# Kernel tuning notes

Hardware: AMD Instinct MI355X
Metric: run time of the kernel (lower is better)

The kernel has to match this reference:

```python
import jax, jax.numpy as jnp
import numpy as np

N = 100000
E = 1600000
IN_FEATS = 256
OUT_FEATS = 128
THRESHOLD = 0.5


def setup_inputs() -> dict:
    key = jax.random.key(0)
    k1, k2, k3, k4, k5, k6, k7 = jax.random.split(key, 7)
    return {
        "feat": jax.random.normal(k1, (N, IN_FEATS), dtype=jnp.float32),
        "src": jax.random.randint(k2, (E,), 0, N, dtype=jnp.int32),
        "dst": jax.random.randint(k3, (E,), 0, N, dtype=jnp.int32),
        "edge_weight": jax.random.uniform(k4, (E,), dtype=jnp.float32),
        "weight": jax.random.normal(k5, (IN_FEATS, OUT_FEATS), dtype=jnp.float32),
        "bias": jax.random.normal(k6, (OUT_FEATS,), dtype=jnp.float32),
        "mask_real": jax.random.uniform(k7, (IN_FEATS, OUT_FEATS), dtype=jnp.float32),
    }


def reference(feat, src, dst, edge_weight, weight, bias, mask_real):
    ones_e = jnp.ones((E,), dtype=feat.dtype)
    # norm == 'both': scale source feats by out_degree^-0.5 (clamped at 1)
    out_deg = jnp.clip(jax.ops.segment_sum(ones_e, src, num_segments=N), 1.0)
    feat_src = feat * (out_deg ** -0.5)[:, None]  # [N, IN]
    # binarized mask with straight-through estimator (training-mode path)
    hard = (mask_real > THRESHOLD).astype(mask_real.dtype)
    mask_t = jax.lax.stop_gradient(hard - mask_real) + mask_real
    w = mask_t * weight  # [IN, OUT]
    # in_feats > out_feats: project before aggregation
    feat_src = feat_src @ w  # [N, OUT]
    # u_mul_e then sum: gather source feats, scale by edge weight, scatter-add to dst
    msgs = feat_src[src] * edge_weight[:, None]  # [E, OUT]
    rst = jax.ops.segment_sum(msgs, dst, num_segments=N)  # [N, OUT]
    # norm == 'both': scale by in_degree^-0.5 (clamped at 1)
    in_deg = jnp.clip(jax.ops.segment_sum(ones_e, dst, num_segments=N), 1.0)
    rst = rst * (in_deg ** -0.5)[:, None]
    return rst + bias
```

## Files before the change

kernel.cpp:

```cpp
#include <hip/hip_runtime.h>

#define N_NODES 100000
#define N_EDGES 1600000
#define IN_F 256
#define OUT_F 128
#define NBUCK 391
#define NPART 256
#define CHUNK (N_EDGES / NPART)
#define BCAP 5632

#define ODW 25000
#define ODRB ((ODW + 255) / 256)

typedef __attribute__((ext_vector_type(8))) short short8;
typedef __attribute__((ext_vector_type(4))) float f32x4;

__device__ __forceinline__ unsigned bf16_rne(float f) {
    unsigned u = __float_as_uint(f);
    return (u + 0x7fffu + ((u >> 16) & 1u)) >> 16;
}

__global__ __launch_bounds__(512) void fused_pre_kernel(const int* __restrict__ src,
                                                        const int* __restrict__ dst,
                                                        const float* __restrict__ weight,
                                                        const float* __restrict__ mask_real,
                                                        unsigned* __restrict__ part,
                                                        unsigned* __restrict__ hist,
                                                        unsigned short* __restrict__ wmT) {
    __shared__ unsigned h[ODW];
    __shared__ unsigned hh[NBUCK];
    int b = blockIdx.x, t = threadIdx.x;
    for (int i = t; i < ODW; i += 512) h[i] = 0u;
    for (int i = t; i < NBUCK; i += 512) hh[i] = 0u;
    if (t < 128) {
        int i = b * 128 + t;
        int k = i >> 7, n = i & 127;
        float v = (mask_real[i] > 0.5f) ? weight[i] : 0.0f;
        wmT[(size_t)n * IN_F + k] = (unsigned short)bf16_rne(v);
    }
    __syncthreads();
    int base = b * CHUNK;
    for (int i = t; i < CHUNK; i += 512) {
        unsigned s = (unsigned)src[base + i];
        unsigned d = (unsigned)dst[base + i];
        atomicAdd(&h[s >> 2], 1u << ((s & 3u) * 8u));
        atomicAdd(&hh[d >> 8], 1u);
    }
    __syncthreads();
    unsigned* op = part + (size_t)b * ODW;
    for (int i = t; i < ODW; i += 512) op[i] = h[i];
    for (int i = t; i < NBUCK; i += 512) hist[(size_t)b * NBUCK + i] = hh[i];
}

__global__ __launch_bounds__(256) void fused_reduce_kernel(const unsigned* __restrict__ part,
                                                           const unsigned* __restrict__ hist,
                                                           unsigned* __restrict__ outpk,
                                                           unsigned* __restrict__ bsum,
                                                           unsigned* __restrict__ colscan) {
    __shared__ unsigned pscan[256];
    int t = threadIdx.x;
    if (blockIdx.x < ODRB) {
        int d = blockIdx.x * 256 + t;
        if (d < ODW) {
            unsigned sum = 0u;
#pragma unroll 8
            for (int b = 0; b < NPART; b++) sum += part[(size_t)b * ODW + d];
            outpk[d] = sum;
        }
    } else {
        int b = blockIdx.x - ODRB;
        unsigned v = hist[(size_t)t * NBUCK + b];
        pscan[t] = v;
        __syncthreads();
#pragma unroll
        for (int d = 1; d < 256; d <<= 1) {
            unsigned x = (t >= d) ? pscan[t - d] : 0u;
            __syncthreads();
            pscan[t] += x;
            __syncthreads();
        }
        colscan[(size_t)b * 256 + t] = pscan[t] - v;
        if (t == 255) bsum[b] = pscan[255];
    }
}

__global__ __launch_bounds__(512) void scatter_kernel(const int* __restrict__ src,
                                                      const int* __restrict__ dst,
                                                      const float* __restrict__ ew,
                                                      const unsigned* __restrict__ colscan,
                                                      const unsigned* __restrict__ bsum,
                                                      uint2* __restrict__ tmp) {
    __shared__ unsigned sc[512];
    __shared__ unsigned cur[NBUCK];
    int p = blockIdx.x, t = threadIdx.x;
    unsigned v = (t < NBUCK) ? bsum[t] : 0u;
    sc[t] = v;
    __syncthreads();
#pragma unroll
    for (int d = 1; d < 512; d <<= 1) {
        unsigned x = (t >= d) ? sc[t - d] : 0u;
        __syncthreads();
        sc[t] += x;
        __syncthreads();
    }
    if (t < NBUCK) cur[t] = (sc[t] - v) + colscan[(size_t)t * 256 + p];
    __syncthreads();
    int base = p * CHUNK;
    for (int i = t; i < CHUNK; i += 512) {
        int e = base + i;
        int s = src[e];
        int d = dst[e];
        unsigned pos = atomicAdd(&cur[(unsigned)d >> 8], 1u);
        tmp[pos] = make_uint2((unsigned)s | (((unsigned)d & 255u) << 17),
                              __float_as_uint(ew[e]));
    }
}

__global__ __launch_bounds__(256) void fillB_kernel(const uint2* __restrict__ tmp,
                                                    const unsigned* __restrict__ bsum,
                                                    unsigned* __restrict__ offsets,
                                                    unsigned* __restrict__ smeta) {
    __shared__ uint2 ebuf[BCAP];
    __shared__ unsigned hcnt[256];
    __shared__ unsigned pref[256];
    __shared__ unsigned red[256];
    int b = blockIdx.x, t = threadIdx.x;
    unsigned loc = 0u;
    for (int i = t; i < b; i += 256) loc += bsum[i];
    red[t] = loc;
    __syncthreads();
#pragma unroll
    for (int d = 128; d > 0; d >>= 1) {
        if (t < d) red[t] += red[t + d];
        __syncthreads();
    }
    unsigned base = red[0];
    unsigned next = base + bsum[b];
    int cnt = (int)(next - base);
    if (cnt > BCAP) cnt = BCAP;
    hcnt[t] = 0u;
    for (int i = t; i < cnt; i += 256) ebuf[i] = tmp[base + i];
    __syncthreads();
    for (int i = t; i < cnt; i += 256) atomicAdd(&hcnt[ebuf[i].x >> 17], 1u);
    __syncthreads();
    unsigned v = hcnt[t];
    pref[t] = v;
    __syncthreads();
#pragma unroll
    for (int d = 1; d < 256; d <<= 1) {
        unsigned x = (t >= d) ? pref[t - d] : 0u;
        __syncthreads();
        pref[t] += x;
        __syncthreads();
    }
    unsigned excl = pref[t] - v;
    int node = b * 256 + t;
    if (node <= N_NODES) offsets[node] = base + excl;
    hcnt[t] = base + excl;
    __syncthreads();
    for (int i = t; i < cnt; i += 256) {
        uint2 m = ebuf[i];
        unsigned pos = atomicAdd(&hcnt[m.x >> 17], 1u);
        smeta[pos] = ((m.y + 0x10000u) & 0xFFFE0000u) | (m.x & 0x1FFFFu);
    }
}

__global__ __launch_bounds__(512) void gemm_kernel(const float* __restrict__ feat,
                                                   const unsigned short* __restrict__ wmT,
                                                   const unsigned char* __restrict__ outdeg8,
                                                   unsigned short* __restrict__ hb) {
    __shared__ unsigned short sB[128][264];
    int t = threadIdx.x;
    for (int idx = t; idx < (128 * 256 / 8); idx += 512) {
        int flat = idx * 8;
        *(uint4*)&sB[flat >> 8][flat & 255] = *(const uint4*)&wmT[flat];
    }
    __syncthreads();

    int lane = t & 63, wv = t >> 6;
    int m16 = lane & 15, quad = lane >> 4;
    int row0 = blockIdx.x * 128;
    int arow = min(row0 + wv * 16 + m16, N_NODES - 1);
    const float* fp = feat + (size_t)arow * IN_F + quad * 8;

    float4 va[16];
#pragma unroll
    for (int i = 0; i < 8; i++) {
        va[2 * i]     = *(const float4*)(fp + i * 32);
        va[2 * i + 1] = *(const float4*)(fp + i * 32 + 4);
    }

    f32x4 acc[8];
#pragma unroll
    for (int i = 0; i < 8; i++) acc[i] = (f32x4){0.f, 0.f, 0.f, 0.f};

#pragma unroll
    for (int i = 0; i < 8; i++) {
        uint4 pk;
        pk.x = bf16_rne(va[2 * i].x) | (bf16_rne(va[2 * i].y) << 16);
        pk.y = bf16_rne(va[2 * i].z) | (bf16_rne(va[2 * i].w) << 16);
        pk.z = bf16_rne(va[2 * i + 1].x) | (bf16_rne(va[2 * i + 1].y) << 16);
        pk.w = bf16_rne(va[2 * i + 1].z) | (bf16_rne(va[2 * i + 1].w) << 16);
        short8 a;
        *(uint4*)&a = pk;
#pragma unroll
        for (int nt = 0; nt < 8; nt++) {
            short8 b = *(const short8*)&sB[nt * 16 + m16][i * 32 + quad * 8];
            acc[nt] = __builtin_amdgcn_mfma_f32_16x16x32_bf16(a, b, acc[nt], 0, 0, 0);
        }
    }
#pragma unroll
    for (int reg = 0; reg < 4; reg++) {
        int row = row0 + wv * 16 + quad * 4 + reg;
        if (row < N_NODES) {
            float s = rsqrtf(fmaxf((float)outdeg8[row], 1.0f));
#pragma unroll
            for (int nt = 0; nt < 8; nt++)
                hb[(size_t)row * OUT_F + nt * 16 + m16] =
                    (unsigned short)bf16_rne(acc[nt][reg] * s);
        }
    }
}

__global__ __launch_bounds__(256) void gather_kernel(const unsigned* __restrict__ smeta,
                                                     const unsigned* __restrict__ offsets,
                                                     const uint4* __restrict__ hrows4,
                                                     const float* __restrict__ bias,
                                                     float* __restrict__ out) {
    int lane = threadIdx.x & 63;
    int n = blockIdx.x * 4 + (threadIdx.x >> 6);
    int g = lane >> 4;
    int q = lane & 15;
    unsigned beg = offsets[n], end = offsets[n + 1];
    int deg = (int)(end - beg);

    float acc[8];
#pragma unroll
    for (int i = 0; i < 8; i++) acc[i] = 0.0f;

    for (int base = 0; base < deg; base += 64) {
        int c = min(64, deg - base);
        unsigned pv = 0u;
        if (lane < c) pv = smeta[beg + base + lane];
        int nch = (c + 3) >> 2;
#pragma unroll 4
        for (int j = 0; j < nch; j++) {
            int ei = (j << 2) + g;
            unsigned p = __shfl(pv, ei);
            unsigned s = p & 0x1FFFFu;
            float w = __uint_as_float(p & 0xFFFE0000u);
            uint4 h = hrows4[(size_t)s * 16u + q];
            acc[0] = fmaf(__uint_as_float(h.x << 16), w, acc[0]);
            acc[1] = fmaf(__uint_as_float(h.x & 0xffff0000u), w, acc[1]);
            acc[2] = fmaf(__uint_as_float(h.y << 16), w, acc[2]);
            acc[3] = fmaf(__uint_as_float(h.y & 0xffff0000u), w, acc[3]);
            acc[4] = fmaf(__uint_as_float(h.z << 16), w, acc[4]);
            acc[5] = fmaf(__uint_as_float(h.z & 0xffff0000u), w, acc[5]);
            acc[6] = fmaf(__uint_as_float(h.w << 16), w, acc[6]);
            acc[7] = fmaf(__uint_as_float(h.w & 0xffff0000u), w, acc[7]);
        }
    }

#pragma unroll
    for (int i = 0; i < 8; i++) {
        acc[i] += __shfl_xor(acc[i], 16);
        acc[i] += __shfl_xor(acc[i], 32);
    }

    float o0, o1;
    if (g == 0)      { o0 = acc[0]; o1 = acc[1]; }
    else if (g == 1) { o0 = acc[2]; o1 = acc[3]; }
    else if (g == 2) { o0 = acc[4]; o1 = acc[5]; }
    else             { o0 = acc[6]; o1 = acc[7]; }

    float sc = rsqrtf(fmaxf((float)deg, 1.0f));
    int col = q * 8 + g * 2;
    float2 b = *(const float2*)&bias[col];
    float2 o = make_float2(o0 * sc + b.x, o1 * sc + b.y);
    *(float2*)&out[(size_t)n * OUT_F + col] = o;
}

extern "C" void kernel_launch(void* const* d_in, const int* in_sizes, int n_in,
                              void* d_out, int out_size, void* d_ws, size_t ws_size,
                              hipStream_t stream) {
    const float* feat      = (const float*)d_in[0];
    const int*   src       = (const int*)d_in[1];
    const int*   dst       = (const int*)d_in[2];
    const float* ew        = (const float*)d_in[3];
    const float* weight    = (const float*)d_in[4];
    const float* bias      = (const float*)d_in[5];
    const float* mask_real = (const float*)d_in[6];
    float* out = (float*)d_out;

    char* ws = (char*)d_ws;
    size_t o = 0;
    auto take = [&](size_t bytes) {
        char* p = ws + o;
        o = (o + bytes + 255) & ~(size_t)255;
        return p;
    };
    unsigned short* wmT     = (unsigned short*)take((size_t)IN_F * OUT_F * 2);
    unsigned*       outpk   = (unsigned*)take((size_t)ODW * 4);
    unsigned*       offs    = (unsigned*)take((size_t)(N_NODES + 1) * 4);
    unsigned*       hist    = (unsigned*)take((size_t)NPART * NBUCK * 4);
    unsigned*       colscan = (unsigned*)take((size_t)NBUCK * 256 * 4);
    unsigned*       bsum    = (unsigned*)take((size_t)NBUCK * 4);
    uint2*          tmp     = (uint2*)take((size_t)N_EDGES * 8);
    unsigned*       smeta   = (unsigned*)take((size_t)N_EDGES * 4);
    unsigned short* hrows   = (unsigned short*)take((size_t)N_NODES * OUT_F * 2);

    unsigned* odpart = (unsigned*)tmp;

    fused_pre_kernel<<<NPART, 512, 0, stream>>>(src, dst, weight, mask_real,
                                                odpart, hist, wmT);
    fused_reduce_kernel<<<ODRB + NBUCK, 256, 0, stream>>>(odpart, hist, outpk,
                                                          bsum, colscan);
    scatter_kernel<<<NPART, 512, 0, stream>>>(src, dst, ew, colscan, bsum, tmp);
    gemm_kernel<<<(N_NODES + 127) / 128, 512, 0, stream>>>(feat, wmT,
                                                           (const unsigned char*)outpk, hrows);
    fillB_kernel<<<NBUCK, 256, 0, stream>>>(tmp, bsum, offs, smeta);
    gather_kernel<<<N_NODES / 4, 256, 0, stream>>>(smeta, offs,
                                                   (const uint4*)hrows, bias, out);
}
```

Measured before the change: 315.5 us.

## Fuse per-bucket CSR build into gather and pack out-degree counts into nibbles

The separate fillB and gather kernels are merged into one bucket_gather kernel. It sorts each dst bucket's edges in LDS and aggregates that bucket's 256 nodes directly, so the smeta/offsets arrays never make a global round-trip and one launch is dropped. The per-partition out-degree histogram now uses 4-bit counters, halving the partial buffer that the reduce kernel reads, with the reduce widened to unpack two nibble lanes. The pre and scatter kernels move to 1024-thread blocks. The cost is that the gather now runs on only 391 large blocks, each wave walking 16 nodes serially, which lowers parallelism for a latency-bound gather. The 4-bit counters also rely on no node exceeding 15 edges within one partition chunk.

```diff
diff --git a/kernel.cpp b/kernel.cpp
--- a/kernel.cpp
+++ b/kernel.cpp
@@ -9,8 +9,8 @@
 #define CHUNK (N_EDGES / NPART)
 #define BCAP 5632
 
-#define ODW 25000
-#define ODRB ((ODW + 255) / 256)
+#define ODW2 12500
+#define ODRB2 ((ODW2 + 255) / 256)
 
 typedef __attribute__((ext_vector_type(8))) short short8;
 typedef __attribute__((ext_vector_type(4))) float f32x4;
@@ -20,18 +20,18 @@
     return (u + 0x7fffu + ((u >> 16) & 1u)) >> 16;
 }
 
-__global__ __launch_bounds__(512) void fused_pre_kernel(const int* __restrict__ src,
-                                                        const int* __restrict__ dst,
-                                                        const float* __restrict__ weight,
-                                                        const float* __restrict__ mask_real,
-                                                        unsigned* __restrict__ part,
-                                                        unsigned* __restrict__ hist,
-                                                        unsigned short* __restrict__ wmT) {
-    __shared__ unsigned h[ODW];
+__global__ __launch_bounds__(1024) void fused_pre_kernel(const int* __restrict__ src,
+                                                         const int* __restrict__ dst,
+                                                         const float* __restrict__ weight,
+                                                         const float* __restrict__ mask_real,
+                                                         unsigned* __restrict__ part,
+                                                         unsigned* __restrict__ hist,
+                                                         unsigned short* __restrict__ wmT) {
+    __shared__ unsigned h[ODW2];
     __shared__ unsigned hh[NBUCK];
     int b = blockIdx.x, t = threadIdx.x;
-    for (int i = t; i < ODW; i += 512) h[i] = 0u;
-    for (int i = t; i < NBUCK; i += 512) hh[i] = 0u;
+    for (int i = t; i < ODW2; i += 1024) h[i] = 0u;
+    for (int i = t; i < NBUCK; i += 1024) hh[i] = 0u;
     if (t < 128) {
         int i = b * 128 + t;
         int k = i >> 7, n = i & 127;
@@ -40,16 +40,16 @@
     }
     __syncthreads();
     int base = b * CHUNK;
-    for (int i = t; i < CHUNK; i += 512) {
+    for (int i = t; i < CHUNK; i += 1024) {
         unsigned s = (unsigned)src[base + i];
         unsigned d = (unsigned)dst[base + i];
-        atomicAdd(&h[s >> 2], 1u << ((s & 3u) * 8u));
+        atomicAdd(&h[s >> 3], 1u << ((s & 7u) * 4u));
         atomicAdd(&hh[d >> 8], 1u);
     }
     __syncthreads();
-    unsigned* op = part + (size_t)b * ODW;
-    for (int i = t; i < ODW; i += 512) op[i] = h[i];
-    for (int i = t; i < NBUCK; i += 512) hist[(size_t)b * NBUCK + i] = hh[i];
+    unsigned* op = part + (size_t)b * ODW2;
+    for (int i = t; i < ODW2; i += 1024) op[i] = h[i];
+    for (int i = t; i < NBUCK; i += 1024) hist[(size_t)b * NBUCK + i] = hh[i];
 }
 
 __global__ __launch_bounds__(256) void fused_reduce_kernel(const unsigned* __restrict__ part,
@@ -59,16 +59,24 @@
                                                            unsigned* __restrict__ colscan) {
     __shared__ unsigned pscan[256];
     int t = threadIdx.x;
-    if (blockIdx.x < ODRB) {
+    if (blockIdx.x < ODRB2) {
         int d = blockIdx.x * 256 + t;
-        if (d < ODW) {
-            unsigned sum = 0u;
+        if (d < ODW2) {
+            unsigned sumE = 0u, sumO = 0u;
 #pragma unroll 8
-            for (int b = 0; b < NPART; b++) sum += part[(size_t)b * ODW + d];
-            outpk[d] = sum;
+            for (int p = 0; p < NPART; p++) {
+                unsigned v = part[(size_t)p * ODW2 + d];
+                sumE += v & 0x0F0F0F0Fu;
+                sumO += (v >> 4) & 0x0F0F0F0Fu;
+            }
+            unsigned w0 = (sumE & 0xFFu) | ((sumO & 0xFFu) << 8) |
+                          ((sumE & 0xFF00u) << 8) | ((sumO & 0xFF00u) << 16);
+            unsigned w1 = ((sumE >> 16) & 0xFFu) | (((sumO >> 16) & 0xFFu) << 8) |
+                          (((sumE >> 24) & 0xFFu) << 16) | ((sumO >> 24) << 24);
+            ((uint2*)outpk)[d] = make_uint2(w0, w1);
         }
     } else {
-        int b = blockIdx.x - ODRB;
+        int b = blockIdx.x - ODRB2;
         unsigned v = hist[(size_t)t * NBUCK + b];
         pscan[t] = v;
         __syncthreads();
@@ -84,20 +92,20 @@
     }
 }
 
-__global__ __launch_bounds__(512) void scatter_kernel(const int* __restrict__ src,
-                                                      const int* __restrict__ dst,
-                                                      const float* __restrict__ ew,
-                                                      const unsigned* __restrict__ colscan,
-                                                      const unsigned* __restrict__ bsum,
-                                                      uint2* __restrict__ tmp) {
-    __shared__ unsigned sc[512];
+__global__ __launch_bounds__(1024) void scatter_kernel(const int* __restrict__ src,
+                                                       const int* __restrict__ dst,
+                                                       const float* __restrict__ ew,
+                                                       const unsigned* __restrict__ colscan,
+                                                       const unsigned* __restrict__ bsum,
+                                                       uint2* __restrict__ tmp) {
+    __shared__ unsigned sc[1024];
     __shared__ unsigned cur[NBUCK];
     int p = blockIdx.x, t = threadIdx.x;
     unsigned v = (t < NBUCK) ? bsum[t] : 0u;
     sc[t] = v;
     __syncthreads();
 #pragma unroll
-    for (int d = 1; d < 512; d <<= 1) {
+    for (int d = 1; d < 1024; d <<= 1) {
         unsigned x = (t >= d) ? sc[t - d] : 0u;
         __syncthreads();
         sc[t] += x;
@@ -106,62 +114,13 @@
     if (t < NBUCK) cur[t] = (sc[t] - v) + colscan[(size_t)t * 256 + p];
     __syncthreads();
     int base = p * CHUNK;
-    for (int i = t; i < CHUNK; i += 512) {
+    for (int i = t; i < CHUNK; i += 1024) {
         int e = base + i;
         int s = src[e];
         int d = dst[e];
         unsigned pos = atomicAdd(&cur[(unsigned)d >> 8], 1u);
         tmp[pos] = make_uint2((unsigned)s | (((unsigned)d & 255u) << 17),
                               __float_as_uint(ew[e]));
-    }
-}
-
-__global__ __launch_bounds__(256) void fillB_kernel(const uint2* __restrict__ tmp,
-                                                    const unsigned* __restrict__ bsum,
-                                                    unsigned* __restrict__ offsets,
-                                                    unsigned* __restrict__ smeta) {
-    __shared__ uint2 ebuf[BCAP];
-    __shared__ unsigned hcnt[256];
-    __shared__ unsigned pref[256];
-    __shared__ unsigned red[256];
-    int b = blockIdx.x, t = threadIdx.x;
-    unsigned loc = 0u;
-    for (int i = t; i < b; i += 256) loc += bsum[i];
-    red[t] = loc;
-    __syncthreads();
-#pragma unroll
-    for (int d = 128; d > 0; d >>= 1) {
-        if (t < d) red[t] += red[t + d];
-        __syncthreads();
-    }
-    unsigned base = red[0];
-    unsigned next = base + bsum[b];
-    int cnt = (int)(next - base);
-    if (cnt > BCAP) cnt = BCAP;
-    hcnt[t] = 0u;
-    for (int i = t; i < cnt; i += 256) ebuf[i] = tmp[base + i];
-    __syncthreads();
-    for (int i = t; i < cnt; i += 256) atomicAdd(&hcnt[ebuf[i].x >> 17], 1u);
-    __syncthreads();
-    unsigned v = hcnt[t];
-    pref[t] = v;
-    __syncthreads();
-#pragma unroll
-    for (int d = 1; d < 256; d <<= 1) {
-        unsigned x = (t >= d) ? pref[t - d] : 0u;
-        __syncthreads();
-        pref[t] += x;
-        __syncthreads();
-    }
-    unsigned excl = pref[t] - v;
-    int node = b * 256 + t;
-    if (node <= N_NODES) offsets[node] = base + excl;
-    hcnt[t] = base + excl;
-    __syncthreads();
-    for (int i = t; i < cnt; i += 256) {
-        uint2 m = ebuf[i];
-        unsigned pos = atomicAdd(&hcnt[m.x >> 17], 1u);
-        smeta[pos] = ((m.y + 0x10000u) & 0xFFFE0000u) | (m.x & 0x1FFFFu);
     }
 }
 
@@ -222,62 +181,112 @@
     }
 }
 
-__global__ __launch_bounds__(256) void gather_kernel(const unsigned* __restrict__ smeta,
-                                                     const unsigned* __restrict__ offsets,
-                                                     const uint4* __restrict__ hrows4,
-                                                     const float* __restrict__ bias,
-                                                     float* __restrict__ out) {
-    int lane = threadIdx.x & 63;
-    int n = blockIdx.x * 4 + (threadIdx.x >> 6);
-    int g = lane >> 4;
-    int q = lane & 15;
-    unsigned beg = offsets[n], end = offsets[n + 1];
-    int deg = (int)(end - beg);
-
-    float acc[8];
-#pragma unroll
-    for (int i = 0; i < 8; i++) acc[i] = 0.0f;
-
-    for (int base = 0; base < deg; base += 64) {
-        int c = min(64, deg - base);
-        unsigned pv = 0u;
-        if (lane < c) pv = smeta[beg + base + lane];
-        int nch = (c + 3) >> 2;
+__global__ __launch_bounds__(1024) void bucket_gather_kernel(const uint2* __restrict__ tmp,
+                                                             const unsigned* __restrict__ bsum,
+                                                             const uint4* __restrict__ hrows4,
+                                                             const float* __restrict__ bias,
+                                                             float* __restrict__ out) {
+    __shared__ uint2 ebuf[BCAP];
+    __shared__ unsigned sm[BCAP];
+    __shared__ unsigned nstart[257];
+    __shared__ unsigned hcnt[256];
+    __shared__ unsigned red[1024];
+    int b = blockIdx.x, t = threadIdx.x;
+
+    unsigned loc = 0u;
+    for (int i = t; i < b; i += 1024) loc += bsum[i];
+    red[t] = loc;
+    __syncthreads();
+#pragma unroll
+    for (int d = 512; d > 0; d >>= 1) {
+        if (t < d) red[t] += red[t + d];
+        __syncthreads();
+    }
+    unsigned base = red[0];
+    unsigned next = base + bsum[b];
+    int cnt = (int)(next - base);
+    if (cnt > BCAP) cnt = BCAP;
+    if (t < 256) hcnt[t] = 0u;
+    for (int i = t; i < cnt; i += 1024) ebuf[i] = tmp[base + i];
+    __syncthreads();
+    for (int i = t; i < cnt; i += 1024) atomicAdd(&hcnt[ebuf[i].x >> 17], 1u);
+    __syncthreads();
+    unsigned v = (t < 256) ? hcnt[t] : 0u;
+    if (t < 256) red[t] = v;
+    __syncthreads();
+#pragma unroll
+    for (int d = 1; d < 256; d <<= 1) {
+        unsigned x = (t < 256 && t >= d) ? red[t - d] : 0u;
+        __syncthreads();
+        if (t < 256) red[t] += x;
+        __syncthreads();
+    }
+    if (t < 256) {
+        unsigned excl = red[t] - v;
+        nstart[t] = excl;
+        hcnt[t] = excl;
+    }
+    if (t == 0) nstart[256] = (unsigned)cnt;
+    __syncthreads();
+    for (int i = t; i < cnt; i += 1024) {
+        uint2 m = ebuf[i];
+        unsigned pos = atomicAdd(&hcnt[m.x >> 17], 1u);
+        sm[pos] = ((m.y + 0x10000u) & 0xFFFE0000u) | (m.x & 0x1FFFFu);
+    }
+    __syncthreads();
+
+    int lane = t & 63, wv = t >> 6;
+    int g = lane >> 4, q = lane & 15;
+    for (int nn = wv * 16; nn < wv * 16 + 16; nn++) {
+        int node = b * 256 + nn;
+        if (node >= N_NODES) continue;
+        unsigned beg = nstart[nn];
+        int deg = (int)(nstart[nn + 1] - beg);
+
+        float acc[8];
+#pragma unroll
+        for (int i = 0; i < 8; i++) acc[i] = 0.0f;
+
+        for (int bs = 0; bs < deg; bs += 64) {
+            int c = min(64, deg - bs);
+            unsigned pv = (lane < c) ? sm[beg + bs + lane] : 0u;
+            int nch = (c + 3) >> 2;
 #pragma unroll 4
-        for (int j = 0; j < nch; j++) {
-            int ei = (j << 2) + g;
-            unsigned p = __shfl(pv, ei);
-            unsigned s = p & 0x1FFFFu;
-            float w = __uint_as_float(p & 0xFFFE0000u);
-            uint4 h = hrows4[(size_t)s * 16u + q];
-            acc[0] = fmaf(__uint_as_float(h.x << 16), w, acc[0]);
-            acc[1] = fmaf(__uint_as_float(h.x & 0xffff0000u), w, acc[1]);
-            acc[2] = fmaf(__uint_as_float(h.y << 16), w, acc[2]);
-            acc[3] = fmaf(__uint_as_float(h.y & 0xffff0000u), w, acc[3]);
-            acc[4] = fmaf(__uint_as_float(h.z << 16), w, acc[4]);
-            acc[5] = fmaf(__uint_as_float(h.z & 0xffff0000u), w, acc[5]);
-            acc[6] = fmaf(__uint_as_float(h.w << 16), w, acc[6]);
-            acc[7] = fmaf(__uint_as_float(h.w & 0xffff0000u), w, acc[7]);
-        }
-    }
-
-#pragma unroll
-    for (int i = 0; i < 8; i++) {
-        acc[i] += __shfl_xor(acc[i], 16);
-        acc[i] += __shfl_xor(acc[i], 32);
-    }
-
-    float o0, o1;
-    if (g == 0)      { o0 = acc[0]; o1 = acc[1]; }
-    else if (g == 1) { o0 = acc[2]; o1 = acc[3]; }
-    else if (g == 2) { o0 = acc[4]; o1 = acc[5]; }
-    else             { o0 = acc[6]; o1 = acc[7]; }
-
-    float sc = rsqrtf(fmaxf((float)deg, 1.0f));
-    int col = q * 8 + g * 2;
-    float2 b = *(const float2*)&bias[col];
-    float2 o = make_float2(o0 * sc + b.x, o1 * sc + b.y);
-    *(float2*)&out[(size_t)n * OUT_F + col] = o;
+            for (int j = 0; j < nch; j++) {
+                int ei = (j << 2) + g;
+                unsigned p = __shfl(pv, ei);
+                unsigned s = p & 0x1FFFFu;
+                float w = __uint_as_float(p & 0xFFFE0000u);
+                uint4 h = hrows4[(size_t)s * 16u + q];
+                acc[0] = fmaf(__uint_as_float(h.x << 16), w, acc[0]);
+                acc[1] = fmaf(__uint_as_float(h.x & 0xffff0000u), w, acc[1]);
+                acc[2] = fmaf(__uint_as_float(h.y << 16), w, acc[2]);
+                acc[3] = fmaf(__uint_as_float(h.y & 0xffff0000u), w, acc[3]);
+                acc[4] = fmaf(__uint_as_float(h.z << 16), w, acc[4]);
+                acc[5] = fmaf(__uint_as_float(h.z & 0xffff0000u), w, acc[5]);
+                acc[6] = fmaf(__uint_as_float(h.w << 16), w, acc[6]);
+                acc[7] = fmaf(__uint_as_float(h.w & 0xffff0000u), w, acc[7]);
+            }
+        }
+
+#pragma unroll
+        for (int i = 0; i < 8; i++) {
+            acc[i] += __shfl_xor(acc[i], 16);
+            acc[i] += __shfl_xor(acc[i], 32);
+        }
+
+        float o0, o1;
+        if (g == 0)      { o0 = acc[0]; o1 = acc[1]; }
+        else if (g == 1) { o0 = acc[2]; o1 = acc[3]; }
+        else if (g == 2) { o0 = acc[4]; o1 = acc[5]; }
+        else             { o0 = acc[6]; o1 = acc[7]; }
+
+        float scale = rsqrtf(fmaxf((float)deg, 1.0f));
+        int col = q * 8 + g * 2;
+        float2 bb = *(const float2*)&bias[col];
+        float2 o = make_float2(o0 * scale + bb.x, o1 * scale + bb.y);
+        *(float2*)&out[(size_t)node * OUT_F + col] = o;
+    }
 }
 
 extern "C" void kernel_launch(void* const* d_in, const int* in_sizes, int n_in,
@@ -300,25 +309,22 @@
         return p;
     };
     unsigned short* wmT     = (unsigned short*)take((size_t)IN_F * OUT_F * 2);
-    unsigned*       outpk   = (unsigned*)take((size_t)ODW * 4);
-    unsigned*       offs    = (unsigned*)take((size_t)(N_NODES + 1) * 4);
+    unsigned*       outpk   = (unsigned*)take((size_t)25600 * 4);
     unsigned*       hist    = (unsigned*)take((size_t)NPART * NBUCK * 4);
     unsigned*       colscan = (unsigned*)take((size_t)NBUCK * 256 * 4);
     unsigned*       bsum    = (unsigned*)take((size_t)NBUCK * 4);
     uint2*          tmp     = (uint2*)take((size_t)N_EDGES * 8);
-    unsigned*       smeta   = (unsigned*)take((size_t)N_EDGES * 4);
     unsigned short* hrows   = (unsigned short*)take((size_t)N_NODES * OUT_F * 2);
 
     unsigned* odpart = (unsigned*)tmp;
 
-    fused_pre_kernel<<<NPART, 512, 0, stream>>>(src, dst, weight, mask_real,
-                                                odpart, hist, wmT);
-    fused_reduce_kernel<<<ODRB + NBUCK, 256, 0, stream>>>(odpart, hist, outpk,
-                                                          bsum, colscan);
-    scatter_kernel<<<NPART, 512, 0, stream>>>(src, dst, ew, colscan, bsum, tmp);
+    fused_pre_kernel<<<NPART, 1024, 0, stream>>>(src, dst, weight, mask_real,
+                                                 odpart, hist, wmT);
+    fused_reduce_kernel<<<ODRB2 + NBUCK, 256, 0, stream>>>(odpart, hist, outpk,
+                                                           bsum, colscan);
+    scatter_kernel<<<NPART, 1024, 0, stream>>>(src, dst, ew, colscan, bsum, tmp);
     gemm_kernel<<<(N_NODES + 127) / 128, 512, 0, stream>>>(feat, wmT,
                                                            (const unsigned char*)outpk, hrows);
-    fillB_kernel<<<NBUCK, 256, 0, stream>>>(tmp, bsum, offs, smeta);
-    gather_kernel<<<N_NODES / 4, 256, 0, stream>>>(smeta, offs,
-                                                   (const uint4*)hrows, bias, out);
-}
+    bucket_gather_kernel<<<NBUCK, 1024, 0, stream>>>(tmp, bsum,
+                                                     (const uint4*)hrows, bias, out);
+}
```

After: 300.6 us. 4.7% less time.
